# Kernel optimization log

Measured on AMD Instinct MI355X. Metric: run time of the kernel, lower is better.

## Reference

```python
import jax, jax.numpy as jnp
import numpy as np

B, T = 8, 256
IDIM = 80; ODIM = 80; HDIM = 256; CDIM = 64
TEMPER = 1.0; ETH = 40.0
N_ITER = HDIM // CDIM  # 4


def shift_windows(key, pad, window):
    # key: (B,T,D) -> all shifted windows (B,T,S,window), S = D + 2*pad - window + 1
    D = key.shape[-1]
    kp = jnp.pad(key, ((0, 0), (0, 0), (pad, pad)))
    S = D + 2 * pad - window + 1
    idx = jnp.arange(S)[:, None] + jnp.arange(window)[None, :]
    return kp[..., idx]


def sim_argmax(x_aug, y):
    # cosine similarity over feature dim, argmax over shift dim S
    num = jnp.einsum('btsw,btw->bts', x_aug, y)
    den = jnp.sqrt(jnp.sum(x_aug ** 2, -1)) * jnp.sqrt(jnp.sum(y ** 2, -1))[..., None] + 1e-6
    sim = num / den
    theta = jnp.argmax(sim, -1)  # (B,T)
    y_al = jnp.take_along_axis(x_aug, theta[..., None, None], 2)[..., 0, :]
    s_opt = jnp.take_along_axis(sim, theta[..., None], -1)[..., 0]
    return y_al, s_opt, theta


def reverse_shift(y_al, pad, window, theta, D):
    # place aligned window back at its original offset (inverse of shift theta)
    yp = jnp.pad(y_al, ((0, 0), (0, 0), (pad, pad)))
    S = window + 2 * pad - D + 1
    idx = jnp.arange(S)[:, None] + jnp.arange(D)[None, :]
    win = yp[..., idx]  # (B,T,S,D)
    start = 2 * pad - theta
    return jnp.take_along_axis(win, start[..., None, None], 2)[..., 0, :]


def attention(x, y, temper):
    return jax.nn.softmax(x * y / temper, axis=-1)


def seq_loss(pred, tgt, mask):
    # elementwise MSE, zeroed at padded positions (mask True)
    return jnp.where(mask, 0.0, (pred - tgt) ** 2)


def hsr(h, mask_prev, seq_mask_t):
    # topk energy masking with cross-iteration exclusivity (hidden-space regularization)
    idx = jax.lax.top_k(h ** 2, CDIM)[1]
    mask_cur = jax.nn.one_hot(idx, HDIM, dtype=h.dtype).sum(-2)
    if mask_prev is None:
        mask_new, loss_h = mask_cur, None
    else:
        inter = mask_prev * mask_cur
        lh = jnp.where(seq_mask_t[..., None], 0.0, (h - (1.0 - inter)) ** 2)
        loss_h = jnp.sum(jnp.where(inter > 0, lh, 0.0))
        h = jnp.where(mask_prev > 0, 0.0, h)
        idx = jax.lax.top_k(h ** 2, CDIM)[1]
        mask_cur = jax.nn.one_hot(idx, HDIM, dtype=h.dtype).sum(-2)
        mask_new = mask_prev + mask_cur
    return h * mask_cur, mask_new, loss_h


def conv1d_encode(z, W, b, D):
    # windowed encoder: all D+1 offsets of a width-2D window, pick max-energy offset
    zw = shift_windows(z, D, 2 * D)                 # (B,T,D+1,2D)
    h = jnp.einsum('btsw,wh->btsh', zw, W) + b      # (B,T,D+1,H)
    ind = jnp.argmax(jnp.sum(h ** 2, -1), -1)       # (B,T)
    h_sel = jnp.take_along_axis(h, ind[..., None, None], 2)[..., 0, :]
    return h_sel, ind


def conv1d_decode(h, W, b, ind, D):
    # gather length-D slice starting at the encoder's chosen offset
    ext = jnp.einsum('bth,hw->btw', h, W) + b       # (B,T,2D)
    idx = ind[..., None] + jnp.arange(D)            # (B,T,D)
    return jnp.take_along_axis(ext, idx, -1)


def _forward(x, y, We, be, Wd, bd, Wds, bds):
    seq_mask = (y == 0.0)                 # ignore_out = 0.0
    seq_mask_t = jnp.all(seq_mask, -1)    # per-timestep padding flag
    y_res, x_res = y, x
    mp_src = mp_self = None
    losses = []
    for _ in range(N_ITER):
        x_aug = shift_windows(x_res, ODIM - 1, ODIM)
        y_al, s_opt, theta = sim_argmax(x_aug, y_res)
        attn = attention(y_al, y_res, TEMPER)
        x_ele = reverse_shift(y_al * attn, ODIM - 1, ODIM, theta, IDIM)
        # self branch (conv1d)
        h_self, ind_self = conv1d_encode(x_ele, We, be, IDIM)
        h_self, mp_self, lh_self = hsr(h_self, mp_self, seq_mask_t)
        x_ele = conv1d_decode(h_self, Wds, bds, ind_self, IDIM)
        move = jnp.abs(theta - IDIM + 1)[..., None]
        ll_self = jnp.where(move > ETH, 0.0, seq_loss(x_ele, x_res, seq_mask)) / (move.astype(x.dtype) + 1.0)
        # re-align decoded x_ele to y_res
        x_aug = shift_windows(x_ele, ODIM - 1, ODIM)
        y_al, s_opt, theta = sim_argmax(x_aug, y_res)
        # src branch (conv1d)
        h_src, ind_src = conv1d_encode(y_al, We, be, IDIM)
        h_src, mp_src, lh_src = hsr(h_src, mp_src, seq_mask_t)
        y_ele = conv1d_decode(h_src, Wd, bd, ind_src, ODIM)
        move = jnp.abs(theta - ODIM + 1)[..., None]
        ll_src = jnp.where(move > ETH, 0.0, seq_loss(y_ele, y_res, seq_mask)) / (move.astype(x.dtype) + 1.0)
        loss_it = ll_src.sum() + ll_self.sum()
        if lh_src is not None:
            loss_it = loss_it + lh_src + lh_self
        losses.append(loss_it)
        y_res = jax.lax.stop_gradient(y_res - y_ele)
        x_res = jax.lax.stop_gradient(x_res - x_ele)
    return jnp.mean(jnp.stack(losses))


def setup_inputs() -> dict:
    key = jax.random.key(0)
    ks = jax.random.split(key, 8)
    return {
        'x': jax.random.normal(ks[0], (B, T, IDIM), jnp.float32),
        'y': jax.random.normal(ks[1], (B, T, ODIM), jnp.float32),
        'We': jax.random.normal(ks[2], (2 * IDIM, HDIM), jnp.float32) * 0.05,
        'be': jnp.zeros((HDIM,), jnp.float32),
        'Wd': jax.random.normal(ks[3], (HDIM, 2 * ODIM), jnp.float32) * 0.05,
        'bd': jnp.zeros((2 * ODIM,), jnp.float32),
        'Wds': jax.random.normal(ks[4], (HDIM, 2 * IDIM), jnp.float32) * 0.05,
        'bds': jnp.zeros((2 * IDIM,), jnp.float32),
    }


def reference(x, y, We, be, Wd, bd, Wds, bds):
    return _forward(x, y, We, be, Wd, bd, Wds, bds)
```

## Files before the change

### kernel.cpp

```cpp
#include <hip/hip_runtime.h>
#include <math.h>

#define NBT 2048

typedef __attribute__((ext_vector_type(8))) short short8;
typedef __attribute__((ext_vector_type(4))) float floatx4;

struct SM {
  alignas(16) float xp[240];
  alignas(16) unsigned xhl[256];
  alignas(16) unsigned long long hkey[256];
  alignas(16) float yres[80];
  alignas(16) float beL[256];
  alignas(16) float spad[240];
  alignas(16) float dval[64];
  alignas(16) int   dlist[64];
  alignas(16) float energyP[4][96];
  float xres[80];
  float yal[80];
  float xele[80];
  float decsrc[80];
  float zb[80];
  float energy[96];
  float mp_self[256];
  float mp_src[256];
  float ext[160];
  unsigned char smask[80];
  int smask_t;
  float abv[4];
  int   abi[4];
  int   wcnt[4];
  float nys;
};

__device__ __forceinline__ float waveSum(float v){
  #pragma unroll
  for (int off = 32; off > 0; off >>= 1) v += __shfl_xor(v, off, 64);
  return v;
}
__device__ __forceinline__ int waveSumI(int v){
  #pragma unroll
  for (int off = 32; off > 0; off >>= 1) v += __shfl_xor(v, off, 64);
  return v;
}
__device__ __forceinline__ float waveMax(float v){
  #pragma unroll
  for (int off = 32; off > 0; off >>= 1) v = fmaxf(v, __shfl_xor(v, off, 64));
  return v;
}

__device__ __forceinline__ int blockArgMax(SM& sm, float v, int idx){
  int lane = threadIdx.x & 63, w = threadIdx.x >> 6;
  #pragma unroll
  for (int off = 32; off > 0; off >>= 1){
    float ov = __shfl_xor(v,   off, 64);
    int   oi = __shfl_xor(idx, off, 64);
    if (ov > v || (ov == v && oi < idx)){ v = ov; idx = oi; }
  }
  if (lane == 0){ sm.abv[w] = v; sm.abi[w] = idx; }
  __syncthreads();
  float bv = sm.abv[0]; int bi = sm.abi[0];
  #pragma unroll
  for (int w2 = 1; w2 < 4; w2++){
    float ov = sm.abv[w2]; int oi = sm.abi[w2];
    if (ov > bv || (ov == bv && oi < bi)){ bv = ov; bi = oi; }
  }
  __syncthreads();
  return bi;
}

__device__ __forceinline__ int rankTop64(SM& sm, unsigned long long mykey){
  int cnt = 0;
  const ulonglong2* q2 = (const ulonglong2*)sm.hkey;
  #pragma unroll 8
  for (int i2 = 0; i2 < 128; i2++){
    ulonglong2 o = q2[i2];
    cnt += (o.x > mykey) ? 1 : 0;
    cnt += (o.y > mykey) ? 1 : 0;
  }
  return (cnt < 64) ? 1 : 0;
}
__device__ __forceinline__ unsigned long long rankKey(float vsq, int j){
  return (((unsigned long long)__float_as_uint(vsq)) << 8)
       | (unsigned long long)(255 - j);
}

__device__ __forceinline__ void compactSel(SM& sm, int sel, float val){
  int tid = threadIdx.x, lane = tid & 63, w = tid >> 6;
  unsigned long long mq = __ballot(sel != 0);
  if (lane == 0) sm.wcnt[w] = __popcll(mq);
  __syncthreads();
  int base = 0;
  #pragma unroll
  for (int i = 0; i < 4; i++) base += (i < w) ? sm.wcnt[i] : 0;
  if (sel){
    unsigned long long below = (lane == 0) ? 0ull : ((~0ull) >> (64 - lane));
    int pos = base + (int)__popcll(mq & below);
    sm.dlist[pos] = tid;
    sm.dval[pos]  = val;
  }
  __syncthreads();
}

__device__ __forceinline__ int simArgmax(SM& sm, const float* src, float* yal_out){
  int tid = threadIdx.x;
  int lane = tid & 63, w = tid >> 6;
  __syncthreads();
  if (tid < 240) sm.spad[tid] = (tid >= 79 && tid < 159) ? src[tid - 79] : 0.f;
  if (w == 0){
    float yv2 = 0.f;
    for (int i = lane; i < 80; i += 64){ float yv = sm.yres[i]; yv2 = fmaf(yv, yv, yv2); }
    float ny = sqrtf(waveSum(yv2));
    if (lane == 0) sm.nys = ny;
  }
  __syncthreads();
  float nys = sm.nys;
  float bv = -INFINITY; int bi = 0;
  if (tid < 159){
    const float4* y4p = (const float4*)sm.yres;
    float num = 0.f, nx = 0.f;
    for (int w4 = 0; w4 < 20; w4++){
      float4 yy = y4p[w4];
      int wb = w4 * 4;
      float xa0 = sm.spad[tid + wb + 0];
      float xa1 = sm.spad[tid + wb + 1];
      float xa2 = sm.spad[tid + wb + 2];
      float xa3 = sm.spad[tid + wb + 3];
      num = fmaf(xa0, yy.x, num); nx = fmaf(xa0, xa0, nx);
      num = fmaf(xa1, yy.y, num); nx = fmaf(xa1, xa1, nx);
      num = fmaf(xa2, yy.z, num); nx = fmaf(xa2, xa2, nx);
      num = fmaf(xa3, yy.w, num); nx = fmaf(xa3, xa3, nx);
    }
    bv = num / (sqrtf(nx) * nys + 1e-6f);
    bi = tid;
  }
  int th = blockArgMax(sm, bv, bi);
  if (tid < 80) yal_out[tid] = sm.spad[th + tid];
  __syncthreads();
  return th;
}

template<int USE_WS>
__device__ __forceinline__ void branchCompute(
    SM& sm, const float* __restrict__ We,
    const short8* __restrict__ wsBh, const short8* __restrict__ wsBl,
    const float* __restrict__ Wdec, const float* __restrict__ bdec,
    const float* enc_in, float* mask, const float* target,
    float* dec_out, int theta, bool first, float& lossAcc)
{
  int tid = threadIdx.x;
  int lane = tid & 63, w = tid >> 6;
  int quad = lane >> 4, l15 = lane & 15;
  __syncthreads();
  {
    float v = (tid >= 80 && tid < 160) ? enc_in[tid - 80] : 0.f;
    if (tid < 240) sm.xp[tid] = v;
    unsigned bits = __float_as_uint(v);
    unsigned hi = bits >> 16;
    float hif = __uint_as_float(hi << 16);
    unsigned lo = __float_as_uint(v - hif) >> 16;
    sm.xhl[tid] = hi | (lo << 16);
  }
  __syncthreads();

  const floatx4 zero4 = {0.f, 0.f, 0.f, 0.f};
  const int ng = w;

  #pragma unroll 1
  for (int mh = 0; mh < 3; mh++){
    int ktlo = (mh == 0) ? 1 : 0;
    int kthi = 5 - mh;
    floatx4 acc[2][4];
    #pragma unroll
    for (int m2 = 0; m2 < 2; m2++)
      #pragma unroll
      for (int nt = 0; nt < 4; nt++) acc[m2][nt] = zero4;

    #pragma unroll 1
    for (int kt = ktlo; kt < kthi; kt++){
      short8 Ah[2], Al[2];
      #pragma unroll
      for (int m2 = 0; m2 < 2; m2++){
        int mt = mh * 2 + m2;
        int base = mt * 16 + l15 + kt * 32 + quad * 8;
        short8 ah, al;
        #pragma unroll
        for (int j = 0; j < 8; j++){
          unsigned u = sm.xhl[base + j];
          ah[j] = (short)(u & 0xffffu);
          al[j] = (short)(u >> 16);
        }
        Ah[m2] = ah; Al[m2] = al;
      }
      #pragma unroll 2
      for (int nt = 0; nt < 4; nt++){
        short8 Bh, Bl;
        int tileIdx = kt * 16 + (ng * 4 + nt);
        if (USE_WS){
          Bh = wsBh[tileIdx * 64 + lane];
          Bl = wsBl[tileIdx * 64 + lane];
        } else {
          short8 bh, bl;
          int k0 = kt * 32 + quad * 8;
          int n  = (ng * 4 + nt) * 16 + l15;
          #pragma unroll
          for (int j = 0; j < 8; j++){
            float v = We[(k0 + j) * 256 + n];
            unsigned bits = __float_as_uint(v);
            unsigned hi = bits >> 16;
            float hif = __uint_as_float(hi << 16);
            unsigned lo = __float_as_uint(v - hif) >> 16;
            bh[j] = (short)hi; bl[j] = (short)lo;
          }
          Bh = bh; Bl = bl;
        }
        acc[0][nt] = __builtin_amdgcn_mfma_f32_16x16x32_bf16(Ah[0], Bh, acc[0][nt], 0, 0, 0);
        acc[0][nt] = __builtin_amdgcn_mfma_f32_16x16x32_bf16(Al[0], Bh, acc[0][nt], 0, 0, 0);
        acc[0][nt] = __builtin_amdgcn_mfma_f32_16x16x32_bf16(Ah[0], Bl, acc[0][nt], 0, 0, 0);
        acc[1][nt] = __builtin_amdgcn_mfma_f32_16x16x32_bf16(Ah[1], Bh, acc[1][nt], 0, 0, 0);
        acc[1][nt] = __builtin_amdgcn_mfma_f32_16x16x32_bf16(Al[1], Bh, acc[1][nt], 0, 0, 0);
        acc[1][nt] = __builtin_amdgcn_mfma_f32_16x16x32_bf16(Ah[1], Bl, acc[1][nt], 0, 0, 0);
      }
    }

    float bn[4];
    #pragma unroll
    for (int nt = 0; nt < 4; nt++) bn[nt] = sm.beL[(ng * 4 + nt) * 16 + l15];
    #pragma unroll
    for (int m2 = 0; m2 < 2; m2++){
      int mt = mh * 2 + m2;
      float er[4];
      #pragma unroll
      for (int r = 0; r < 4; r++){
        float s_ = 0.f;
        #pragma unroll
        for (int nt = 0; nt < 4; nt++){
          float hvv = acc[m2][nt][r] + bn[nt];
          s_ = fmaf(hvv, hvv, s_);
        }
        er[r] = s_;
      }
      #pragma unroll
      for (int x2 = 1; x2 < 16; x2 <<= 1){
        #pragma unroll
        for (int r = 0; r < 4; r++) er[r] += __shfl_xor(er[r], x2, 64);
      }
      if (l15 == 0){
        #pragma unroll
        for (int r = 0; r < 4; r++)
          sm.energyP[w][mt * 16 + quad * 4 + r] = er[r];
      }
    }
  }
  __syncthreads();
  if (tid < 96){
    float e = sm.energyP[0][tid];
    e += sm.energyP[1][tid];
    e += sm.energyP[2][tid];
    e += sm.energyP[3][tid];
    sm.energy[tid] = e;
  }
  __syncthreads();

  float bvE = (tid < 81) ? sm.energy[tid] : -INFINITY;
  int   biE = (tid < 81) ? tid : 0;
  int ind = blockArgMax(sm, bvE, biE);

  int roff = 80 - ind;
  float hv = sm.beL[tid];
  #pragma unroll 4
  for (int w2 = 0; w2 < 80; w2++){
    float xv = sm.xp[80 + w2];
    hv = fmaf(xv, We[(w2 + roff) * 256 + tid], hv);
  }

  float vsq = hv * hv;
  unsigned long long myk = rankKey(vsq, tid);
  sm.hkey[tid] = myk;
  __syncthreads();
  int sel1 = rankTop64(sm, myk);
  float mpv = mask[tid];
  if (first){
    mask[tid] = (float)sel1;
    compactSel(sm, sel1, hv);
  } else {
    int st = sm.smask_t;
    float interv = mpv * (float)sel1;
    if (interv > 0.f && !st){
      float dd = hv - (1.f - interv);
      lossAcc += dd * dd;
    }
    float h2 = (mpv > 0.f) ? 0.f : hv;
    __syncthreads();
    unsigned long long myk2 = rankKey(h2 * h2, tid);
    sm.hkey[tid] = myk2;
    __syncthreads();
    int sel2 = rankTop64(sm, myk2);
    mask[tid] = mpv + (float)sel2;
    compactSel(sm, sel2, h2);
  }

  if (tid < 160){
    float a = bdec[tid];
    #pragma unroll 8
    for (int i = 0; i < 64; i++){
      int idx = sm.dlist[i];
      float hval = sm.dval[i];
      a = fmaf(hval, Wdec[idx * 160 + tid], a);
    }
    sm.ext[tid] = a;
  }
  __syncthreads();

  float mv = fabsf((float)(theta - 79));
  bool gate = (mv > 40.0f);
  if (tid < 80){
    float dec = sm.ext[ind + tid];
    dec_out[tid] = dec;
    float diff = dec - target[tid];
    float l = (gate || sm.smask[tid]) ? 0.f : diff * diff;
    lossAcc += l / (mv + 1.0f);
  }
  __syncthreads();
}

__global__ void __launch_bounds__(64) zero_out_kernel(float* out){
  if (threadIdx.x == 0) out[0] = 0.f;
}

__global__ void __launch_bounds__(64) prep_we_kernel(
    const float* __restrict__ We, short8* __restrict__ bh, short8* __restrict__ bl){
  int tile = blockIdx.x;
  int lane = threadIdx.x;
  int kt = tile >> 4, nt = tile & 15;
  int k0 = kt * 32 + (lane >> 4) * 8;
  int n  = nt * 16 + (lane & 15);
  short8 h, l;
  #pragma unroll
  for (int j = 0; j < 8; j++){
    float v = We[(k0 + j) * 256 + n];
    unsigned bits = __float_as_uint(v);
    unsigned hi = bits >> 16;
    float hif = __uint_as_float(hi << 16);
    unsigned lo = __float_as_uint(v - hif) >> 16;
    h[j] = (short)hi; l[j] = (short)lo;
  }
  bh[tile * 64 + lane] = h;
  bl[tile * 64 + lane] = l;
}

template<int USE_WS>
__global__ void __launch_bounds__(256, 4) net_kernel(
    const float* __restrict__ x,  const float* __restrict__ y,
    const float* __restrict__ We, const float* __restrict__ be,
    const float* __restrict__ Wd, const float* __restrict__ bd,
    const float* __restrict__ Wds,const float* __restrict__ bds,
    const short8* __restrict__ wsBh, const short8* __restrict__ wsBl,
    float* out)
{
  __shared__ SM sm;
  int tid = threadIdx.x;
  int lane = tid & 63, w = tid >> 6;
  int bt  = blockIdx.x;
  const float* xin = x + bt * 80;
  const float* yin = y + bt * 80;

  if (tid < 80){
    sm.xres[tid] = xin[tid];
    float yv = yin[tid];
    sm.yres[tid] = yv;
    sm.smask[tid] = (yv == 0.f) ? 1 : 0;
  }
  sm.mp_self[tid] = 0.f;
  sm.mp_src[tid]  = 0.f;
  sm.beL[tid] = be[tid];
  __syncthreads();
  if (w == 0){
    int c = 0;
    for (int i = lane; i < 80; i += 64) c += (int)sm.smask[i];
    int total = waveSumI(c);
    if (lane == 0) sm.smask_t = (total == 80) ? 1 : 0;
  }
  __syncthreads();

  float lossAcc = 0.f;

  for (int it = 0; it < 4; it++){
    bool first = (it == 0);

    int th1 = simArgmax(sm, sm.xres, sm.yal);

    if (w == 0){
      float p0 = sm.yal[lane] * sm.yres[lane];
      float p1 = (lane < 16) ? sm.yal[64 + lane] * sm.yres[64 + lane] : -INFINITY;
      float mx = waveMax(fmaxf(p0, p1));
      float e0 = expf(p0 - mx);
      float e1 = (lane < 16) ? expf(p1 - mx) : 0.f;
      float ssum = waveSum(e0 + e1);
      sm.zb[lane] = sm.yal[lane] * (e0 / ssum);
      if (lane < 16) sm.zb[64 + lane] = sm.yal[64 + lane] * (e1 / ssum);
    }
    __syncthreads();

    if (tid < 80){
      int q = tid + 79 - th1;
      sm.xele[tid] = (q >= 0 && q < 80) ? sm.zb[q] : 0.f;
    }

    branchCompute<USE_WS>(sm, We, wsBh, wsBl, Wds, bds,
                          sm.xele, sm.mp_self, sm.xres, sm.xele, th1, first, lossAcc);

    int th2 = simArgmax(sm, sm.xele, sm.yal);

    branchCompute<USE_WS>(sm, We, wsBh, wsBl, Wd, bd,
                          sm.yal, sm.mp_src, sm.yres, sm.decsrc, th2, first, lossAcc);

    __syncthreads();
    if (tid < 80){
      sm.xres[tid] -= sm.xele[tid];
      sm.yres[tid] -= sm.decsrc[tid];
    }
    __syncthreads();
  }

  float vsum = waveSum(lossAcc);
  if (lane == 0) sm.abv[w] = vsum;
  __syncthreads();
  if (tid == 0){
    float total = ((sm.abv[0] + sm.abv[1]) + sm.abv[2]) + sm.abv[3];
    atomicAdd(out, total * 0.25f);
  }
}

extern "C" void kernel_launch(void* const* d_in, const int* in_sizes, int n_in,
                              void* d_out, int out_size, void* d_ws, size_t ws_size,
                              hipStream_t stream) {
  const float* x   = (const float*)d_in[0];
  const float* y   = (const float*)d_in[1];
  const float* We  = (const float*)d_in[2];
  const float* be  = (const float*)d_in[3];
  const float* Wd  = (const float*)d_in[4];
  const float* bd  = (const float*)d_in[5];
  const float* Wds = (const float*)d_in[6];
  const float* bds = (const float*)d_in[7];
  float* out = (float*)d_out;

  const size_t fragCount = 80 * 64;
  const size_t fragBytes = fragCount * sizeof(short8);
  int use_ws = (ws_size >= 2 * fragBytes) ? 1 : 0;
  short8* wsBh = (short8*)d_ws;
  short8* wsBl = wsBh + fragCount;

  hipLaunchKernelGGL(zero_out_kernel, dim3(1), dim3(64), 0, stream, out);
  if (use_ws){
    hipLaunchKernelGGL(prep_we_kernel, dim3(80), dim3(64), 0, stream, We, wsBh, wsBl);
    hipLaunchKernelGGL((net_kernel<1>), dim3(NBT), dim3(256), 0, stream,
                       x, y, We, be, Wd, bd, Wds, bds, wsBh, wsBl, out);
  } else {
    hipLaunchKernelGGL((net_kernel<0>), dim3(NBT), dim3(256), 0, stream,
                       x, y, We, be, Wd, bd, Wds, bds, wsBh, wsBl, out);
  }
}
```

Baseline: 672.9 us.

## Store shifted bf16 hi/lo input copies for vector LDS A-fragment loads

The packed hi/lo input array in shared memory becomes eight pre-shifted copies of separate hi and lo short arrays, so each MFMA A-fragment is a single 16-byte LDS load instead of eight scalar loads plus unpacking. The hi/lo weight fragments are interleaved in the workspace so adjacent lanes read both halves from neighbouring addresses. Selected index/value pairs are packed into one int2. The redundant norm recomputation in the second similarity argmax is skipped, and one unroll factor rises. The cost is extra LDS footprint and eight-way stores when building the shifted copies.

```diff
diff --git a/kernel.cpp b/kernel.cpp
--- a/kernel.cpp
+++ b/kernel.cpp
@@ -8,13 +8,13 @@
 
 struct SM {
   alignas(16) float xp[240];
-  alignas(16) unsigned xhl[256];
+  alignas(16) short xhr[8][264];
+  alignas(16) short xlr[8][264];
   alignas(16) unsigned long long hkey[256];
   alignas(16) float yres[80];
   alignas(16) float beL[256];
   alignas(16) float spad[240];
-  alignas(16) float dval[64];
-  alignas(16) int   dlist[64];
+  alignas(16) int2  dpair[64];
   alignas(16) float energyP[4][96];
   float xres[80];
   float yal[80];
@@ -96,18 +96,17 @@
   if (sel){
     unsigned long long below = (lane == 0) ? 0ull : ((~0ull) >> (64 - lane));
     int pos = base + (int)__popcll(mq & below);
-    sm.dlist[pos] = tid;
-    sm.dval[pos]  = val;
-  }
-  __syncthreads();
-}
-
-__device__ __forceinline__ int simArgmax(SM& sm, const float* src, float* yal_out){
+    sm.dpair[pos] = make_int2(tid, __float_as_int(val));
+  }
+  __syncthreads();
+}
+
+__device__ __forceinline__ int simArgmax(SM& sm, const float* src, float* yal_out, int doNy){
   int tid = threadIdx.x;
   int lane = tid & 63, w = tid >> 6;
   __syncthreads();
   if (tid < 240) sm.spad[tid] = (tid >= 79 && tid < 159) ? src[tid - 79] : 0.f;
-  if (w == 0){
+  if (doNy && w == 0){
     float yv2 = 0.f;
     for (int i = lane; i < 80; i += 64){ float yv = sm.yres[i]; yv2 = fmaf(yv, yv, yv2); }
     float ny = sqrtf(waveSum(yv2));
@@ -143,7 +142,7 @@
 template<int USE_WS>
 __device__ __forceinline__ void branchCompute(
     SM& sm, const float* __restrict__ We,
-    const short8* __restrict__ wsBh, const short8* __restrict__ wsBl,
+    const short8* __restrict__ wsB,
     const float* __restrict__ Wdec, const float* __restrict__ bdec,
     const float* enc_in, float* mask, const float* target,
     float* dec_out, int theta, bool first, float& lossAcc)
@@ -159,12 +158,19 @@
     unsigned hi = bits >> 16;
     float hif = __uint_as_float(hi << 16);
     unsigned lo = __float_as_uint(v - hif) >> 16;
-    sm.xhl[tid] = hi | (lo << 16);
+    short hs = (short)hi, ls = (short)lo;
+    #pragma unroll
+    for (int c = 0; c < 8; c++){
+      int i = tid - c;
+      if (i >= 0){ sm.xhr[c][i] = hs; sm.xlr[c][i] = ls; }
+    }
   }
   __syncthreads();
 
   const floatx4 zero4 = {0.f, 0.f, 0.f, 0.f};
   const int ng = w;
+  const int c8 = l15 & 7;
+  const int hb = l15 >> 3;
 
   #pragma unroll 1
   for (int mh = 0; mh < 3; mh++){
@@ -182,23 +188,18 @@
       #pragma unroll
       for (int m2 = 0; m2 < 2; m2++){
         int mt = mh * 2 + m2;
-        int base = mt * 16 + l15 + kt * 32 + quad * 8;
-        short8 ah, al;
-        #pragma unroll
-        for (int j = 0; j < 8; j++){
-          unsigned u = sm.xhl[base + j];
-          ah[j] = (short)(u & 0xffffu);
-          al[j] = (short)(u >> 16);
-        }
-        Ah[m2] = ah; Al[m2] = al;
+        int kb = quad + 2 * mt + 4 * kt + hb;
+        Ah[m2] = *reinterpret_cast<const short8*>(&sm.xhr[c8][8 * kb]);
+        Al[m2] = *reinterpret_cast<const short8*>(&sm.xlr[c8][8 * kb]);
       }
       #pragma unroll 2
       for (int nt = 0; nt < 4; nt++){
         short8 Bh, Bl;
         int tileIdx = kt * 16 + (ng * 4 + nt);
         if (USE_WS){
-          Bh = wsBh[tileIdx * 64 + lane];
-          Bl = wsBl[tileIdx * 64 + lane];
+          int ti2 = (tileIdx * 64 + lane) * 2;
+          Bh = wsB[ti2];
+          Bl = wsB[ti2 + 1];
         } else {
           short8 bh, bl;
           int k0 = kt * 32 + quad * 8;
@@ -268,7 +269,7 @@
 
   int roff = 80 - ind;
   float hv = sm.beL[tid];
-  #pragma unroll 4
+  #pragma unroll 8
   for (int w2 = 0; w2 < 80; w2++){
     float xv = sm.xp[80 + w2];
     hv = fmaf(xv, We[(w2 + roff) * 256 + tid], hv);
@@ -304,9 +305,8 @@
     float a = bdec[tid];
     #pragma unroll 8
     for (int i = 0; i < 64; i++){
-      int idx = sm.dlist[i];
-      float hval = sm.dval[i];
-      a = fmaf(hval, Wdec[idx * 160 + tid], a);
+      int2 p = sm.dpair[i];
+      a = fmaf(__int_as_float(p.y), Wdec[p.x * 160 + tid], a);
     }
     sm.ext[tid] = a;
   }
@@ -329,7 +329,7 @@
 }
 
 __global__ void __launch_bounds__(64) prep_we_kernel(
-    const float* __restrict__ We, short8* __restrict__ bh, short8* __restrict__ bl){
+    const float* __restrict__ We, short8* __restrict__ wsB){
   int tile = blockIdx.x;
   int lane = threadIdx.x;
   int kt = tile >> 4, nt = tile & 15;
@@ -345,8 +345,9 @@
     unsigned lo = __float_as_uint(v - hif) >> 16;
     h[j] = (short)hi; l[j] = (short)lo;
   }
-  bh[tile * 64 + lane] = h;
-  bl[tile * 64 + lane] = l;
+  int ti2 = (tile * 64 + lane) * 2;
+  wsB[ti2]     = h;
+  wsB[ti2 + 1] = l;
 }
 
 template<int USE_WS>
@@ -355,7 +356,7 @@
     const float* __restrict__ We, const float* __restrict__ be,
     const float* __restrict__ Wd, const float* __restrict__ bd,
     const float* __restrict__ Wds,const float* __restrict__ bds,
-    const short8* __restrict__ wsBh, const short8* __restrict__ wsBl,
+    const short8* __restrict__ wsB,
     float* out)
 {
   __shared__ SM sm;
@@ -388,7 +389,7 @@
   for (int it = 0; it < 4; it++){
     bool first = (it == 0);
 
-    int th1 = simArgmax(sm, sm.xres, sm.yal);
+    int th1 = simArgmax(sm, sm.xres, sm.yal, 1);
 
     if (w == 0){
       float p0 = sm.yal[lane] * sm.yres[lane];
@@ -407,12 +408,12 @@
       sm.xele[tid] = (q >= 0 && q < 80) ? sm.zb[q] : 0.f;
     }
 
-    branchCompute<USE_WS>(sm, We, wsBh, wsBl, Wds, bds,
+    branchCompute<USE_WS>(sm, We, wsB, Wds, bds,
                           sm.xele, sm.mp_self, sm.xres, sm.xele, th1, first, lossAcc);
 
-    int th2 = simArgmax(sm, sm.xele, sm.yal);
-
-    branchCompute<USE_WS>(sm, We, wsBh, wsBl, Wd, bd,
+    int th2 = simArgmax(sm, sm.xele, sm.yal, 0);
+
+    branchCompute<USE_WS>(sm, We, wsB, Wd, bd,
                           sm.yal, sm.mp_src, sm.yres, sm.decsrc, th2, first, lossAcc);
 
     __syncthreads();
@@ -445,19 +446,18 @@
   const float* bds = (const float*)d_in[7];
   float* out = (float*)d_out;
 
-  const size_t fragCount = 80 * 64;
+  const size_t fragCount = 80 * 64 * 2;
   const size_t fragBytes = fragCount * sizeof(short8);
-  int use_ws = (ws_size >= 2 * fragBytes) ? 1 : 0;
-  short8* wsBh = (short8*)d_ws;
-  short8* wsBl = wsBh + fragCount;
+  int use_ws = (ws_size >= fragBytes) ? 1 : 0;
+  short8* wsB = (short8*)d_ws;
 
   hipLaunchKernelGGL(zero_out_kernel, dim3(1), dim3(64), 0, stream, out);
   if (use_ws){
-    hipLaunchKernelGGL(prep_we_kernel, dim3(80), dim3(64), 0, stream, We, wsBh, wsBl);
+    hipLaunchKernelGGL(prep_we_kernel, dim3(80), dim3(64), 0, stream, We, wsB);
     hipLaunchKernelGGL((net_kernel<1>), dim3(NBT), dim3(256), 0, stream,
-                       x, y, We, be, Wd, bd, Wds, bds, wsBh, wsBl, out);
+                       x, y, We, be, Wd, bd, Wds, bds, wsB, out);
   } else {
     hipLaunchKernelGGL((net_kernel<0>), dim3(NBT), dim3(256), 0, stream,
-                       x, y, We, be, Wd, bd, Wds, bds, wsBh, wsBl, out);
-  }
-}
+                       x, y, We, be, Wd, bd, Wds, bds, wsB, out);
+  }
+}
```

Result: faster. 641.5 us (-4.7%).
